# Optimization experiments

Hardware: AMD Instinct MI355X
Metric: run time of the kernel (lower is better)

The kernel has to match this reference:

```python
import jax, jax.numpy as jnp
import numpy as np

N = 100000          # nodes
E = 1600000         # edges (avg degree 16)
IN_DIM = 32
HID = 64
K = 2
XH = IN_DIM + HID   # 96, DiffConv input dim


def _xavier(key, shape):
    fan_in, fan_out = shape[-2], shape[-1]
    lim = float(np.sqrt(6.0 / (fan_in + fan_out)))
    return jax.random.uniform(key, shape, jnp.float32, -lim, lim)


def setup_inputs() -> dict:
    key = jax.random.key(0)
    ks = jax.random.split(key, 8)
    x = jax.random.normal(ks[0], (N, IN_DIM), jnp.float32)
    h = jax.random.normal(ks[1], (N, HID), jnp.float32)
    edge_index = jax.random.randint(ks[2], (2, E), 0, N, dtype=jnp.int32)
    edge_weight = jax.random.uniform(ks[3], (E,), jnp.float32)
    # stacked per-hop linear weights for each gate: (K+1, XH, HID)
    Wr = _xavier(ks[4], (K + 1, XH, HID))
    Wz = _xavier(ks[5], (K + 1, XH, HID))
    Wc = _xavier(ks[6], (K + 1, XH, HID))
    br = jnp.zeros((HID,), jnp.float32)
    bz = jnp.zeros((HID,), jnp.float32)
    bc = jnp.zeros((HID,), jnp.float32)
    return {"x": x, "h": h, "edge_index": edge_index, "edge_weight": edge_weight,
            "Wr": Wr, "br": br, "Wz": Wz, "bz": bz, "Wc": Wc, "bc": bc}


def _diff_conv(x, src, dst, norm_w, W, b, n):
    # DC(X) = sum_k Linear_k(P^k X),  P = D^{-1} W (row-normalised)
    out = x @ W[0]
    x_k = x
    for k in range(1, W.shape[0]):
        msgs = norm_w[:, None] * x_k[src]                     # gather + scale (E, F)
        x_k = jax.ops.segment_sum(msgs, dst, num_segments=n)  # scatter-add (N, F)
        out = out + x_k @ W[k]
    return out + b


def reference(x, h, edge_index, edge_weight, Wr, br, Wz, bz, Wc, bc):
    n = x.shape[0]
    src, dst = edge_index[0], edge_index[1]
    # out-degree normalisation on source nodes (clamped at 1)
    out_deg = jax.ops.segment_sum(jnp.ones_like(edge_weight), src, num_segments=n)
    out_deg = jnp.maximum(out_deg, 1.0)
    norm_w = edge_weight / out_deg[src]
    xh = jnp.concatenate([x, h], axis=-1)
    r = jax.nn.sigmoid(_diff_conv(xh, src, dst, norm_w, Wr, br, n))
    z = jax.nn.sigmoid(_diff_conv(xh, src, dst, norm_w, Wz, bz, n))
    xrh = jnp.concatenate([x, r * h], axis=-1)
    c = jnp.tanh(_diff_conv(xrh, src, dst, norm_w, Wc, bc, n))
    return z * h + (1.0 - z) * c
```

## Files before the change

kernel.cpp:

```cpp
#include <hip/hip_runtime.h>
#include <math.h>

#define NN 100000
#define NE 1600000
#define ECAP 64
#define GN 64
#define WSTR 296
#define LSTR 104

#define EPB 4096
#define NBLKA 391
#define BINB 256
#define NBINS 391
#define BCAP 4736

typedef __attribute__((ext_vector_type(4))) float f32x4;
typedef __attribute__((ext_vector_type(8))) short s16x8;

__device__ __forceinline__ unsigned int bfbits(float v) {
  unsigned int b = __float_as_uint(v);
  b += 0x7fffu + ((b >> 16) & 1u);
  return b >> 16;
}
__device__ __forceinline__ float bflo(unsigned int v) { return __uint_as_float(v << 16); }
__device__ __forceinline__ float bfhi(unsigned int v) { return __uint_as_float(v & 0xffff0000u); }
__device__ __forceinline__ uint4 pack8(float4 a, float4 b) {
  return make_uint4(bfbits(a.x) | (bfbits(a.y) << 16), bfbits(a.z) | (bfbits(a.w) << 16),
                    bfbits(b.x) | (bfbits(b.y) << 16), bfbits(b.z) | (bfbits(b.w) << 16));
}

__global__ __launch_bounds__(256) void k_binA(const int* __restrict__ src,
                                              const int* __restrict__ dst,
                                              const float* __restrict__ ew,
                                              int* __restrict__ gcur1,
                                              int* __restrict__ gcur2,
                                              int2* __restrict__ rec1,
                                              unsigned char* __restrict__ rec2) {
  __shared__ int h1[NBINS], h2[NBINS];
  int tid = threadIdx.x;
  for (int t = tid; t < NBINS; t += 256) { h1[t] = 0; h2[t] = 0; }
  __syncthreads();
  int base = blockIdx.x * EPB;
  int end = base + EPB; if (end > NE) end = NE;
  for (int e = base + tid; e < end; e += 256) {
    atomicAdd(&h1[dst[e] >> 8], 1);
    atomicAdd(&h2[src[e] >> 8], 1);
  }
  __syncthreads();
  for (int t = tid; t < NBINS; t += 256) {
    int c1 = h1[t];
    h1[t] = t * BCAP + (c1 ? atomicAdd(&gcur1[t], c1) : 0);
    int c2 = h2[t];
    h2[t] = t * BCAP + (c2 ? atomicAdd(&gcur2[t], c2) : 0);
  }
  __syncthreads();
  for (int e = base + tid; e < end; e += 256) {
    int d = dst[e], s = src[e];
    int p1 = atomicAdd(&h1[d >> 8], 1);
    rec1[p1] = make_int2(s | ((d & 255) << 20), __float_as_int(ew[e]));
    int p2 = atomicAdd(&h2[s >> 8], 1);
    rec2[p2] = (unsigned char)(s & 255);
  }
}

__global__ __launch_bounds__(256) void k_bdeg(const int* __restrict__ gcur2,
                                              const unsigned char* __restrict__ rec2,
                                              int* __restrict__ deg_out) {
  __shared__ int lc[BINB];
  int b = blockIdx.x, tid = threadIdx.x;
  lc[tid] = 0;
  __syncthreads();
  int cnt = gcur2[b];
  const unsigned char* rp = rec2 + (size_t)b * BCAP;
  for (int i = tid; i < cnt; i += 256) atomicAdd(&lc[rp[i]], 1);
  __syncthreads();
  int node = b * 256 + tid;
  if (node < NN) deg_out[node] = lc[tid];
}

__global__ __launch_bounds__(256) void k_bell(const int* __restrict__ gcur1,
                                              const int2* __restrict__ rec1,
                                              const int* __restrict__ deg_out,
                                              int2* __restrict__ ell,
                                              int* __restrict__ cursor) {
  __shared__ int lc[BINB];
  int b = blockIdx.x, tid = threadIdx.x;
  lc[tid] = 0;
  __syncthreads();
  int cnt = gcur1[b];
  const int2* rp = rec1 + (size_t)b * BCAP;
  for (int i = tid; i < cnt; i += 256) {
    int2 r = rp[i];
    int s = r.x & 0xFFFFF;
    int dl = (r.x >> 20) & 255;
    float w = __int_as_float(r.y) / fmaxf((float)deg_out[s], 1.0f);
    int p = atomicAdd(&lc[dl], 1);
    if (p < ECAP)
      ell[(size_t)(b * 256 + dl) * ECAP + p] = make_int2(s, __float_as_int(w));
  }
  __syncthreads();
  int node = b * 256 + tid;
  if (node < NN) cursor[node] = lc[tid];
}

__global__ __launch_bounds__(256) void k_xh0(const float* __restrict__ x,
                                             const float* __restrict__ h,
                                             unsigned int* __restrict__ xh0) {
  int idx = blockIdx.x * 256 + threadIdx.x;
  if (idx >= NN * 48) return;
  int n = idx / 48, c = idx - n * 48;
  float v0, v1;
  if (c < 16) {
    v0 = x[(size_t)n * 32 + 2 * c];
    v1 = x[(size_t)n * 32 + 2 * c + 1];
  } else {
    v0 = h[(size_t)n * 64 + 2 * (c - 16)];
    v1 = h[(size_t)n * 64 + 2 * (c - 16) + 1];
  }
  xh0[idx] = bfbits(v0) | (bfbits(v1) << 16);
}

__global__ __launch_bounds__(256) void k_wprep(const float* __restrict__ Wr,
                                               const float* __restrict__ Wz,
                                               const float* __restrict__ Wc,
                                               unsigned short* __restrict__ wt_rz,
                                               unsigned short* __restrict__ wt_c) {
  int idx = blockIdx.x * 256 + threadIdx.x;
  if (idx >= 192 * 36) return;
  int col = idx % 192;
  int k0 = (idx / 192) * 8;
  unsigned int packed[4];
#pragma unroll
  for (int p = 0; p < 4; ++p) {
    unsigned int lo, hi;
#pragma unroll
    for (int e = 0; e < 2; ++e) {
      int k = k0 + p * 2 + e;
      int t = k / 96, kl = k - t * 96;
      float v;
      if (col < 64) v = Wr[t * 6144 + kl * 64 + col];
      else if (col < 128) v = Wz[t * 6144 + kl * 64 + (col - 64)];
      else v = Wc[t * 6144 + kl * 64 + (col - 128)];
      if (e == 0) lo = bfbits(v); else hi = bfbits(v);
    }
    packed[p] = lo | (hi << 16);
  }
  unsigned short* dstp = (col < 128) ? (wt_rz + col * WSTR + k0)
                                     : (wt_c + (col - 128) * WSTR + k0);
  *reinterpret_cast<uint4*>(dstp) =
      make_uint4(packed[0], packed[1], packed[2], packed[3]);
}

__global__ __launch_bounds__(256) void k_prop96e(const uint2* __restrict__ in,
                                                 uint2* __restrict__ out,
                                                 const int* __restrict__ cnt_arr,
                                                 const int2* __restrict__ ell) {
  int hw = (blockIdx.x * 256 + threadIdx.x) >> 5;
  int lane = threadIdx.x & 31;
  if (hw >= NN) return;
  int cnt = cnt_arr[hw];
  if (cnt > ECAP) cnt = ECAP;
  const int2* ep = ell + (size_t)hw * ECAP;
  bool act = lane < 24;
  float a0 = 0.f, a1 = 0.f, a2 = 0.f, a3 = 0.f;
  float b0 = 0.f, b1 = 0.f, b2 = 0.f, b3 = 0.f;
  int i = 0;
  for (; i + 4 <= cnt; i += 4) {
    int2 e0 = ep[i], e1 = ep[i + 1], e2 = ep[i + 2], e3 = ep[i + 3];
    if (act) {
      uint2 v0 = in[(size_t)e0.x * 24 + lane];
      uint2 v1 = in[(size_t)e1.x * 24 + lane];
      uint2 v2 = in[(size_t)e2.x * 24 + lane];
      uint2 v3 = in[(size_t)e3.x * 24 + lane];
      float w0 = __int_as_float(e0.y), w1 = __int_as_float(e1.y);
      float w2 = __int_as_float(e2.y), w3 = __int_as_float(e3.y);
      a0 = fmaf(w0, bflo(v0.x), a0); a1 = fmaf(w0, bfhi(v0.x), a1);
      a2 = fmaf(w0, bflo(v0.y), a2); a3 = fmaf(w0, bfhi(v0.y), a3);
      b0 = fmaf(w1, bflo(v1.x), b0); b1 = fmaf(w1, bfhi(v1.x), b1);
      b2 = fmaf(w1, bflo(v1.y), b2); b3 = fmaf(w1, bfhi(v1.y), b3);
      a0 = fmaf(w2, bflo(v2.x), a0); a1 = fmaf(w2, bfhi(v2.x), a1);
      a2 = fmaf(w2, bflo(v2.y), a2); a3 = fmaf(w2, bfhi(v2.y), a3);
      b0 = fmaf(w3, bflo(v3.x), b0); b1 = fmaf(w3, bfhi(v3.x), b1);
      b2 = fmaf(w3, bflo(v3.y), b2); b3 = fmaf(w3, bfhi(v3.y), b3);
    }
  }
  for (; i < cnt; ++i) {
    int2 e = ep[i];
    if (act) {
      uint2 v = in[(size_t)e.x * 24 + lane];
      float w = __int_as_float(e.y);
      a0 = fmaf(w, bflo(v.x), a0); a1 = fmaf(w, bfhi(v.x), a1);
      a2 = fmaf(w, bflo(v.y), a2); a3 = fmaf(w, bfhi(v.y), a3);
    }
  }
  if (act) {
    uint2 o;
    o.x = bfbits(a0 + b0) | (bfbits(a1 + b1) << 16);
    o.y = bfbits(a2 + b2) | (bfbits(a3 + b3) << 16);
    out[(size_t)hw * 24 + lane] = o;
  }
}

__global__ __launch_bounds__(256) void k_prop64e(const unsigned int* __restrict__ in,
                                                 unsigned int* __restrict__ out,
                                                 const int* __restrict__ cnt_arr,
                                                 const int2* __restrict__ ell) {
  int hw = (blockIdx.x * 256 + threadIdx.x) >> 5;
  int lane = threadIdx.x & 31;
  if (hw >= NN) return;
  int cnt = cnt_arr[hw];
  if (cnt > ECAP) cnt = ECAP;
  const int2* ep = ell + (size_t)hw * ECAP;
  float a0 = 0.f, a1 = 0.f, b0 = 0.f, b1 = 0.f;
  int i = 0;
  for (; i + 4 <= cnt; i += 4) {
    int2 e0 = ep[i], e1 = ep[i + 1], e2 = ep[i + 2], e3 = ep[i + 3];
    unsigned int v0 = in[(size_t)e0.x * 32 + lane];
    unsigned int v1 = in[(size_t)e1.x * 32 + lane];
    unsigned int v2 = in[(size_t)e2.x * 32 + lane];
    unsigned int v3 = in[(size_t)e3.x * 32 + lane];
    float w0 = __int_as_float(e0.y), w1 = __int_as_float(e1.y);
    float w2 = __int_as_float(e2.y), w3 = __int_as_float(e3.y);
    a0 = fmaf(w0, bflo(v0), a0); a1 = fmaf(w0, bfhi(v0), a1);
    b0 = fmaf(w1, bflo(v1), b0); b1 = fmaf(w1, bfhi(v1), b1);
    a0 = fmaf(w2, bflo(v2), a0); a1 = fmaf(w2, bfhi(v2), a1);
    b0 = fmaf(w3, bflo(v3), b0); b1 = fmaf(w3, bfhi(v3), b1);
  }
  for (; i < cnt; ++i) {
    int2 e = ep[i];
    unsigned int v = in[(size_t)e.x * 32 + lane];
    float w = __int_as_float(e.y);
    a0 = fmaf(w, bflo(v), a0); a1 = fmaf(w, bfhi(v), a1);
  }
  out[(size_t)hw * 32 + lane] = bfbits(a0 + b0) | (bfbits(a1 + b1) << 16);
}

__device__ __forceinline__ void stage_f32f32(unsigned short* sA, int nb0,
                                             const float* __restrict__ srcA,
                                             const float* __restrict__ srcB) {
  for (int i = threadIdx.x; i < GN * 12; i += 256) {
    int n = i / 12, ch = i % 12;
    int g = nb0 + n;
    uint4 v = make_uint4(0, 0, 0, 0);
    if (g < NN) {
      if (ch < 4) {
        float4 f0 = *reinterpret_cast<const float4*>(srcA + (size_t)g * 32 + ch * 8);
        float4 f1 = *reinterpret_cast<const float4*>(srcA + (size_t)g * 32 + ch * 8 + 4);
        v = pack8(f0, f1);
      } else {
        float4 f0 = *reinterpret_cast<const float4*>(srcB + (size_t)g * 64 + (ch - 4) * 8);
        float4 f1 = *reinterpret_cast<const float4*>(srcB + (size_t)g * 64 + (ch - 4) * 8 + 4);
        v = pack8(f0, f1);
      }
    }
    *reinterpret_cast<uint4*>(&sA[n * LSTR + ch * 8]) = v;
  }
}

__device__ __forceinline__ void stage_copy96(unsigned short* sA, int nb0,
                                             const unsigned short* __restrict__ src) {
  for (int i = threadIdx.x; i < GN * 12; i += 256) {
    int n = i / 12, ch = i % 12;
    int g = nb0 + n;
    uint4 v = make_uint4(0, 0, 0, 0);
    if (g < NN) v = *reinterpret_cast<const uint4*>(src + (size_t)g * 96 + ch * 8);
    *reinterpret_cast<uint4*>(&sA[n * LSTR + ch * 8]) = v;
  }
}

__device__ __forceinline__ void stage_f32bf(unsigned short* sA, int nb0,
                                            const float* __restrict__ srcA,
                                            const unsigned short* __restrict__ srcB) {
  for (int i = threadIdx.x; i < GN * 12; i += 256) {
    int n = i / 12, ch = i % 12;
    int g = nb0 + n;
    uint4 v = make_uint4(0, 0, 0, 0);
    if (g < NN) {
      if (ch < 4) {
        float4 f0 = *reinterpret_cast<const float4*>(srcA + (size_t)g * 32 + ch * 8);
        float4 f1 = *reinterpret_cast<const float4*>(srcA + (size_t)g * 32 + ch * 8 + 4);
        v = pack8(f0, f1);
      } else {
        v = *reinterpret_cast<const uint4*>(srcB + (size_t)g * 64 + (ch - 4) * 8);
      }
    }
    *reinterpret_cast<uint4*>(&sA[n * LSTR + ch * 8]) = v;
  }
}

__device__ __forceinline__ void stage_bfbf(unsigned short* sA, int nb0,
                                           const unsigned short* __restrict__ srcA,
                                           const unsigned short* __restrict__ srcB) {
  for (int i = threadIdx.x; i < GN * 12; i += 256) {
    int n = i / 12, ch = i % 12;
    int g = nb0 + n;
    uint4 v = make_uint4(0, 0, 0, 0);
    if (g < NN) {
      if (ch < 4) v = *reinterpret_cast<const uint4*>(srcA + (size_t)g * 96 + ch * 8);
      else v = *reinterpret_cast<const uint4*>(srcB + (size_t)g * 64 + (ch - 4) * 8);
    }
    *reinterpret_cast<uint4*>(&sA[n * LSTR + ch * 8]) = v;
  }
}

template <int NCOLS>
__device__ __forceinline__ void stage_w(unsigned short* sW,
                                        const unsigned short* __restrict__ wt, int t) {
  for (int i = threadIdx.x; i < NCOLS * 12; i += 256) {
    int col = i / 12, ch = i % 12;
    uint4 v = *reinterpret_cast<const uint4*>(wt + col * WSTR + t * 96 + ch * 8);
    *reinterpret_cast<uint4*>(&sW[col * LSTR + ch * 8]) = v;
  }
}

__global__ __launch_bounds__(256) void k_rz(const float* __restrict__ x,
                                            const float* __restrict__ h,
                                            const unsigned short* __restrict__ xh1,
                                            const unsigned short* __restrict__ xh2,
                                            const unsigned short* __restrict__ wt_rz,
                                            const float* __restrict__ br,
                                            const float* __restrict__ bz,
                                            unsigned short* __restrict__ rh,
                                            float* __restrict__ zb) {
  __shared__ alignas(16) unsigned short sA[GN * LSTR];
  __shared__ alignas(16) unsigned short sW[128 * LSTR];
  int tid = threadIdx.x;
  int nb0 = blockIdx.x * GN;
  int wv = tid >> 6, l = tid & 63;
  int l15 = l & 15, lg = l >> 4;
  int n0 = wv * 32;

  f32x4 acc[4][2];
#pragma unroll
  for (int nt = 0; nt < 2; ++nt) {
    int colc = n0 + nt * 16 + l15;
    float bias = (colc < 64) ? br[colc] : bz[colc - 64];
#pragma unroll
    for (int mt = 0; mt < 4; ++mt) acc[mt][nt] = {bias, bias, bias, bias};
  }

#pragma unroll
  for (int t = 0; t < 3; ++t) {
    if (t == 0) stage_f32f32(sA, nb0, x, h);
    else if (t == 1) stage_copy96(sA, nb0, xh1);
    else stage_copy96(sA, nb0, xh2);
    stage_w<128>(sW, wt_rz, t);
    __syncthreads();
#pragma unroll
    for (int ks = 0; ks < 3; ++ks) {
      int kb = ks * 32 + lg * 8;
      s16x8 af[4];
#pragma unroll
      for (int mt = 0; mt < 4; ++mt)
        af[mt] = *reinterpret_cast<const s16x8*>(&sA[(mt * 16 + l15) * LSTR + kb]);
      s16x8 bf0 = *reinterpret_cast<const s16x8*>(&sW[(n0 + l15) * LSTR + kb]);
      s16x8 bf1 = *reinterpret_cast<const s16x8*>(&sW[(n0 + 16 + l15) * LSTR + kb]);
#pragma unroll
      for (int mt = 0; mt < 4; ++mt) {
        acc[mt][0] = __builtin_amdgcn_mfma_f32_16x16x32_bf16(af[mt], bf0, acc[mt][0], 0, 0, 0);
        acc[mt][1] = __builtin_amdgcn_mfma_f32_16x16x32_bf16(af[mt], bf1, acc[mt][1], 0, 0, 0);
      }
    }
    __syncthreads();
  }

#pragma unroll
  for (int mt = 0; mt < 4; ++mt) {
#pragma unroll
    for (int nt = 0; nt < 2; ++nt) {
      int colc = n0 + nt * 16 + l15;
#pragma unroll
      for (int r = 0; r < 4; ++r) {
        int g = nb0 + mt * 16 + lg * 4 + r;
        if (g < NN) {
          float pre = acc[mt][nt][r];
          float sg = 1.f / (1.f + expf(-pre));
          if (colc < 64) {
            float hv = h[(size_t)g * 64 + colc];
            rh[(size_t)g * 64 + colc] = (unsigned short)bfbits(sg * hv);
          } else {
            zb[(size_t)g * 64 + (colc - 64)] = sg;
          }
        }
      }
    }
  }
}

__global__ __launch_bounds__(256) void k_c(const float* __restrict__ x,
                                           const float* __restrict__ h,
                                           const unsigned short* __restrict__ rhf,
                                           const unsigned short* __restrict__ xh1,
                                           const unsigned short* __restrict__ xh2,
                                           const unsigned short* __restrict__ rh1,
                                           const unsigned short* __restrict__ rh2,
                                           const unsigned short* __restrict__ wt_c,
                                           const float* __restrict__ bc,
                                           const float* __restrict__ zb,
                                           float* __restrict__ out) {
  __shared__ alignas(16) unsigned short sA[GN * LSTR];
  __shared__ alignas(16) unsigned short sW[64 * LSTR];
  int tid = threadIdx.x;
  int nb0 = blockIdx.x * GN;
  int wv = tid >> 6, l = tid & 63;
  int l15 = l & 15, lg = l >> 4;
  int n0 = wv * 16;

  float bias = bc[n0 + l15];
  f32x4 acc[4];
#pragma unroll
  for (int mt = 0; mt < 4; ++mt) acc[mt] = {bias, bias, bias, bias};

#pragma unroll
  for (int t = 0; t < 3; ++t) {
    if (t == 0) stage_f32bf(sA, nb0, x, rhf);
    else if (t == 1) stage_bfbf(sA, nb0, xh1, rh1);
    else stage_bfbf(sA, nb0, xh2, rh2);
    stage_w<64>(sW, wt_c, t);
    __syncthreads();
#pragma unroll
    for (int ks = 0; ks < 3; ++ks) {
      int kb = ks * 32 + lg * 8;
      s16x8 bf0 = *reinterpret_cast<const s16x8*>(&sW[(n0 + l15) * LSTR + kb]);
#pragma unroll
      for (int mt = 0; mt < 4; ++mt) {
        s16x8 af = *reinterpret_cast<const s16x8*>(&sA[(mt * 16 + l15) * LSTR + kb]);
        acc[mt] = __builtin_amdgcn_mfma_f32_16x16x32_bf16(af, bf0, acc[mt], 0, 0, 0);
      }
    }
    __syncthreads();
  }

  int colc = n0 + l15;
#pragma unroll
  for (int mt = 0; mt < 4; ++mt) {
#pragma unroll
    for (int r = 0; r < 4; ++r) {
      int g = nb0 + mt * 16 + lg * 4 + r;
      if (g < NN) {
        float cv = tanhf(acc[mt][r]);
        float z = zb[(size_t)g * 64 + colc];
        float hv = h[(size_t)g * 64 + colc];
        out[(size_t)g * 64 + colc] = z * hv + (1.f - z) * cv;
      }
    }
  }
}

extern "C" void kernel_launch(void* const* d_in, const int* in_sizes, int n_in,
                              void* d_out, int out_size, void* d_ws, size_t ws_size,
                              hipStream_t stream) {
  const float* x = (const float*)d_in[0];
  const float* h = (const float*)d_in[1];
  const int* eidx = (const int*)d_in[2];
  const float* ew = (const float*)d_in[3];
  const float* Wr = (const float*)d_in[4];
  const float* br = (const float*)d_in[5];
  const float* Wz = (const float*)d_in[6];
  const float* bz = (const float*)d_in[7];
  const float* Wc = (const float*)d_in[8];
  const float* bc = (const float*)d_in[9];
  const int* src = eidx;
  const int* dst = eidx + NE;
  float* out = (float*)d_out;

  int* ip = (int*)d_ws;
  int* gcur1 = ip;
  int* gcur2 = ip + 512;
  int* deg_out = ip + 1024;
  int* cursor = deg_out + NN;
  int2* rec1 = (int2*)(cursor + NN);
  unsigned char* rec2 = (unsigned char*)(rec1 + (size_t)NBINS * BCAP);
  int2* ell = (int2*)(rec2 + ((size_t)NBINS * BCAP + 8) / 8 * 8);
  float* zb = (float*)(ell + (size_t)NN * ECAP);
  unsigned short* xh0 = (unsigned short*)(zb + (size_t)NN * 64);
  unsigned short* xh1 = xh0 + (size_t)NN * 96;
  unsigned short* xh2 = xh1 + (size_t)NN * 96;
  unsigned short* rh  = xh2 + (size_t)NN * 96;
  unsigned short* rh1 = rh + (size_t)NN * 64;
  unsigned short* rh2 = rh1 + (size_t)NN * 64;
  unsigned short* wt_rz = rh2 + (size_t)NN * 64;
  unsigned short* wt_c = wt_rz + 128 * WSTR;

  hipMemsetAsync(ip, 0, 1024 * sizeof(int), stream);

  dim3 blk(256);
  k_wprep<<<dim3((192 * 36 + 255) / 256), blk, 0, stream>>>(Wr, Wz, Wc, wt_rz, wt_c);
  k_binA<<<dim3(NBLKA), blk, 0, stream>>>(src, dst, ew, gcur1, gcur2, rec1, rec2);
  k_bdeg<<<dim3(NBINS), blk, 0, stream>>>(gcur2, rec2, deg_out);
  k_bell<<<dim3(NBINS), blk, 0, stream>>>(gcur1, rec1, deg_out, ell, cursor);
  k_xh0<<<dim3(NN * 48 / 256), blk, 0, stream>>>(x, h, (unsigned int*)xh0);

  k_prop96e<<<dim3(NN / 8), blk, 0, stream>>>((const uint2*)xh0, (uint2*)xh1,
                                              cursor, ell);
  k_prop96e<<<dim3(NN / 8), blk, 0, stream>>>((const uint2*)xh1, (uint2*)xh2,
                                              cursor, ell);
  k_rz<<<dim3((NN + GN - 1) / GN), blk, 0, stream>>>(x, h, xh1, xh2, wt_rz, br, bz, rh, zb);
  k_prop64e<<<dim3(NN / 8), blk, 0, stream>>>((const unsigned int*)rh,
                                              (unsigned int*)rh1, cursor, ell);
  k_prop64e<<<dim3(NN / 8), blk, 0, stream>>>((const unsigned int*)rh1,
                                              (unsigned int*)rh2, cursor, ell);
  k_c<<<dim3((NN + GN - 1) / GN), blk, 0, stream>>>(x, h, rh, xh1, xh2, rh1, rh2,
                                                    wt_c, bc, zb, out);
}
```

Before: 426.7 us.

## Read bf16 xh0 and weights directly from global, store z gate in bf16

The gate kernels now stage the precomputed bf16 xh0 buffer instead of re-reading and converting fp32 x and h. Weight fragments are loaded straight from global memory (cached) instead of being staged into shared memory, which drops the sW arrays and lowers LDS use. The z gate is stored as bf16, halving its write and read traffic. The final blend now uses bf16-rounded h and z values, which adds precision loss, and the direct weight loads rely on the cache to keep latency down.

Result: faster. 387.5 us (-9.2%).

```diff
diff --git a/kernel.cpp b/kernel.cpp
--- a/kernel.cpp
+++ b/kernel.cpp
@@ -24,10 +24,7 @@
 }
 __device__ __forceinline__ float bflo(unsigned int v) { return __uint_as_float(v << 16); }
 __device__ __forceinline__ float bfhi(unsigned int v) { return __uint_as_float(v & 0xffff0000u); }
-__device__ __forceinline__ uint4 pack8(float4 a, float4 b) {
-  return make_uint4(bfbits(a.x) | (bfbits(a.y) << 16), bfbits(a.z) | (bfbits(a.w) << 16),
-                    bfbits(b.x) | (bfbits(b.y) << 16), bfbits(b.z) | (bfbits(b.w) << 16));
-}
+__device__ __forceinline__ float bf1(unsigned short v) { return __uint_as_float((unsigned int)v << 16); }
 
 __global__ __launch_bounds__(256) void k_binA(const int* __restrict__ src,
                                               const int* __restrict__ dst,
@@ -235,28 +232,6 @@
   out[(size_t)hw * 32 + lane] = bfbits(a0 + b0) | (bfbits(a1 + b1) << 16);
 }
 
-__device__ __forceinline__ void stage_f32f32(unsigned short* sA, int nb0,
-                                             const float* __restrict__ srcA,
-                                             const float* __restrict__ srcB) {
-  for (int i = threadIdx.x; i < GN * 12; i += 256) {
-    int n = i / 12, ch = i % 12;
-    int g = nb0 + n;
-    uint4 v = make_uint4(0, 0, 0, 0);
-    if (g < NN) {
-      if (ch < 4) {
-        float4 f0 = *reinterpret_cast<const float4*>(srcA + (size_t)g * 32 + ch * 8);
-        float4 f1 = *reinterpret_cast<const float4*>(srcA + (size_t)g * 32 + ch * 8 + 4);
-        v = pack8(f0, f1);
-      } else {
-        float4 f0 = *reinterpret_cast<const float4*>(srcB + (size_t)g * 64 + (ch - 4) * 8);
-        float4 f1 = *reinterpret_cast<const float4*>(srcB + (size_t)g * 64 + (ch - 4) * 8 + 4);
-        v = pack8(f0, f1);
-      }
-    }
-    *reinterpret_cast<uint4*>(&sA[n * LSTR + ch * 8]) = v;
-  }
-}
-
 __device__ __forceinline__ void stage_copy96(unsigned short* sA, int nb0,
                                              const unsigned short* __restrict__ src) {
   for (int i = threadIdx.x; i < GN * 12; i += 256) {
@@ -264,26 +239,6 @@
     int g = nb0 + n;
     uint4 v = make_uint4(0, 0, 0, 0);
     if (g < NN) v = *reinterpret_cast<const uint4*>(src + (size_t)g * 96 + ch * 8);
-    *reinterpret_cast<uint4*>(&sA[n * LSTR + ch * 8]) = v;
-  }
-}
-
-__device__ __forceinline__ void stage_f32bf(unsigned short* sA, int nb0,
-                                            const float* __restrict__ srcA,
-                                            const unsigned short* __restrict__ srcB) {
-  for (int i = threadIdx.x; i < GN * 12; i += 256) {
-    int n = i / 12, ch = i % 12;
-    int g = nb0 + n;
-    uint4 v = make_uint4(0, 0, 0, 0);
-    if (g < NN) {
-      if (ch < 4) {
-        float4 f0 = *reinterpret_cast<const float4*>(srcA + (size_t)g * 32 + ch * 8);
-        float4 f1 = *reinterpret_cast<const float4*>(srcA + (size_t)g * 32 + ch * 8 + 4);
-        v = pack8(f0, f1);
-      } else {
-        v = *reinterpret_cast<const uint4*>(srcB + (size_t)g * 64 + (ch - 4) * 8);
-      }
-    }
     *reinterpret_cast<uint4*>(&sA[n * LSTR + ch * 8]) = v;
   }
 }
@@ -303,27 +258,15 @@
   }
 }
 
-template <int NCOLS>
-__device__ __forceinline__ void stage_w(unsigned short* sW,
-                                        const unsigned short* __restrict__ wt, int t) {
-  for (int i = threadIdx.x; i < NCOLS * 12; i += 256) {
-    int col = i / 12, ch = i % 12;
-    uint4 v = *reinterpret_cast<const uint4*>(wt + col * WSTR + t * 96 + ch * 8);
-    *reinterpret_cast<uint4*>(&sW[col * LSTR + ch * 8]) = v;
-  }
-}
-
-__global__ __launch_bounds__(256) void k_rz(const float* __restrict__ x,
-                                            const float* __restrict__ h,
+__global__ __launch_bounds__(256) void k_rz(const unsigned short* __restrict__ xh0,
                                             const unsigned short* __restrict__ xh1,
                                             const unsigned short* __restrict__ xh2,
                                             const unsigned short* __restrict__ wt_rz,
                                             const float* __restrict__ br,
                                             const float* __restrict__ bz,
                                             unsigned short* __restrict__ rh,
-                                            float* __restrict__ zb) {
+                                            unsigned short* __restrict__ zbb) {
   __shared__ alignas(16) unsigned short sA[GN * LSTR];
-  __shared__ alignas(16) unsigned short sW[128 * LSTR];
   int tid = threadIdx.x;
   int nb0 = blockIdx.x * GN;
   int wv = tid >> 6, l = tid & 63;
@@ -339,26 +282,25 @@
     for (int mt = 0; mt < 4; ++mt) acc[mt][nt] = {bias, bias, bias, bias};
   }
 
+  const unsigned short* w0p = wt_rz + (size_t)(n0 + l15) * WSTR + lg * 8;
+  const unsigned short* w1p = wt_rz + (size_t)(n0 + 16 + l15) * WSTR + lg * 8;
+
 #pragma unroll
   for (int t = 0; t < 3; ++t) {
-    if (t == 0) stage_f32f32(sA, nb0, x, h);
+    if (t == 0) stage_copy96(sA, nb0, xh0);
     else if (t == 1) stage_copy96(sA, nb0, xh1);
     else stage_copy96(sA, nb0, xh2);
-    stage_w<128>(sW, wt_rz, t);
     __syncthreads();
 #pragma unroll
     for (int ks = 0; ks < 3; ++ks) {
       int kb = ks * 32 + lg * 8;
-      s16x8 af[4];
-#pragma unroll
-      for (int mt = 0; mt < 4; ++mt)
-        af[mt] = *reinterpret_cast<const s16x8*>(&sA[(mt * 16 + l15) * LSTR + kb]);
-      s16x8 bf0 = *reinterpret_cast<const s16x8*>(&sW[(n0 + l15) * LSTR + kb]);
-      s16x8 bf1 = *reinterpret_cast<const s16x8*>(&sW[(n0 + 16 + l15) * LSTR + kb]);
+      s16x8 bf0 = *reinterpret_cast<const s16x8*>(w0p + t * 96 + ks * 32);
+      s16x8 bf1 = *reinterpret_cast<const s16x8*>(w1p + t * 96 + ks * 32);
 #pragma unroll
       for (int mt = 0; mt < 4; ++mt) {
-        acc[mt][0] = __builtin_amdgcn_mfma_f32_16x16x32_bf16(af[mt], bf0, acc[mt][0], 0, 0, 0);
-        acc[mt][1] = __builtin_amdgcn_mfma_f32_16x16x32_bf16(af[mt], bf1, acc[mt][1], 0, 0, 0);
+        s16x8 af = *reinterpret_cast<const s16x8*>(&sA[(mt * 16 + l15) * LSTR + kb]);
+        acc[mt][0] = __builtin_amdgcn_mfma_f32_16x16x32_bf16(af, bf0, acc[mt][0], 0, 0, 0);
+        acc[mt][1] = __builtin_amdgcn_mfma_f32_16x16x32_bf16(af, bf1, acc[mt][1], 0, 0, 0);
       }
     }
     __syncthreads();
@@ -376,10 +318,10 @@
           float pre = acc[mt][nt][r];
           float sg = 1.f / (1.f + expf(-pre));
           if (colc < 64) {
-            float hv = h[(size_t)g * 64 + colc];
+            float hv = bf1(xh0[(size_t)g * 96 + 32 + colc]);
             rh[(size_t)g * 64 + colc] = (unsigned short)bfbits(sg * hv);
           } else {
-            zb[(size_t)g * 64 + (colc - 64)] = sg;
+            zbb[(size_t)g * 64 + (colc - 64)] = (unsigned short)bfbits(sg);
           }
         }
       }
@@ -387,8 +329,7 @@
   }
 }
 
-__global__ __launch_bounds__(256) void k_c(const float* __restrict__ x,
-                                           const float* __restrict__ h,
+__global__ __launch_bounds__(256) void k_c(const unsigned short* __restrict__ xh0,
                                            const unsigned short* __restrict__ rhf,
                                            const unsigned short* __restrict__ xh1,
                                            const unsigned short* __restrict__ xh2,
@@ -396,10 +337,9 @@
                                            const unsigned short* __restrict__ rh2,
                                            const unsigned short* __restrict__ wt_c,
                                            const float* __restrict__ bc,
-                                           const float* __restrict__ zb,
+                                           const unsigned short* __restrict__ zbb,
                                            float* __restrict__ out) {
   __shared__ alignas(16) unsigned short sA[GN * LSTR];
-  __shared__ alignas(16) unsigned short sW[64 * LSTR];
   int tid = threadIdx.x;
   int nb0 = blockIdx.x * GN;
   int wv = tid >> 6, l = tid & 63;
@@ -411,17 +351,18 @@
 #pragma unroll
   for (int mt = 0; mt < 4; ++mt) acc[mt] = {bias, bias, bias, bias};
 
+  const unsigned short* wp = wt_c + (size_t)(n0 + l15) * WSTR + lg * 8;
+
 #pragma unroll
   for (int t = 0; t < 3; ++t) {
-    if (t == 0) stage_f32bf(sA, nb0, x, rhf);
+    if (t == 0) stage_bfbf(sA, nb0, xh0, rhf);
     else if (t == 1) stage_bfbf(sA, nb0, xh1, rh1);
     else stage_bfbf(sA, nb0, xh2, rh2);
-    stage_w<64>(sW, wt_c, t);
     __syncthreads();
 #pragma unroll
     for (int ks = 0; ks < 3; ++ks) {
       int kb = ks * 32 + lg * 8;
-      s16x8 bf0 = *reinterpret_cast<const s16x8*>(&sW[(n0 + l15) * LSTR + kb]);
+      s16x8 bf0 = *reinterpret_cast<const s16x8*>(wp + t * 96 + ks * 32);
 #pragma unroll
       for (int mt = 0; mt < 4; ++mt) {
         s16x8 af = *reinterpret_cast<const s16x8*>(&sA[(mt * 16 + l15) * LSTR + kb]);
@@ -439,8 +380,8 @@
       int g = nb0 + mt * 16 + lg * 4 + r;
       if (g < NN) {
         float cv = tanhf(acc[mt][r]);
-        float z = zb[(size_t)g * 64 + colc];
-        float hv = h[(size_t)g * 64 + colc];
+        float z = bf1(zbb[(size_t)g * 64 + colc]);
+        float hv = bf1(xh0[(size_t)g * 96 + 32 + colc]);
         out[(size_t)g * 64 + colc] = z * hv + (1.f - z) * cv;
       }
     }
@@ -472,8 +413,8 @@
   int2* rec1 = (int2*)(cursor + NN);
   unsigned char* rec2 = (unsigned char*)(rec1 + (size_t)NBINS * BCAP);
   int2* ell = (int2*)(rec2 + ((size_t)NBINS * BCAP + 8) / 8 * 8);
-  float* zb = (float*)(ell + (size_t)NN * ECAP);
-  unsigned short* xh0 = (unsigned short*)(zb + (size_t)NN * 64);
+  unsigned short* zbb = (unsigned short*)(ell + (size_t)NN * ECAP);
+  unsigned short* xh0 = zbb + (size_t)NN * 64;
   unsigned short* xh1 = xh0 + (size_t)NN * 96;
   unsigned short* xh2 = xh1 + (size_t)NN * 96;
   unsigned short* rh  = xh2 + (size_t)NN * 96;
@@ -495,11 +436,11 @@
                                               cursor, ell);
   k_prop96e<<<dim3(NN / 8), blk, 0, stream>>>((const uint2*)xh1, (uint2*)xh2,
                                               cursor, ell);
-  k_rz<<<dim3((NN + GN - 1) / GN), blk, 0, stream>>>(x, h, xh1, xh2, wt_rz, br, bz, rh, zb);
+  k_rz<<<dim3((NN + GN - 1) / GN), blk, 0, stream>>>(xh0, xh1, xh2, wt_rz, br, bz, rh, zbb);
   k_prop64e<<<dim3(NN / 8), blk, 0, stream>>>((const unsigned int*)rh,
                                               (unsigned int*)rh1, cursor, ell);
   k_prop64e<<<dim3(NN / 8), blk, 0, stream>>>((const unsigned int*)rh1,
                                               (unsigned int*)rh2, cursor, ell);
-  k_c<<<dim3((NN + GN - 1) / GN), blk, 0, stream>>>(x, h, rh, xh1, xh2, rh1, rh2,
-                                                    wt_c, bc, zb, out);
-}
+  k_c<<<dim3((NN + GN - 1) / GN), blk, 0, stream>>>(xh0, rh, xh1, xh2, rh1, rh2,
+                                                    wt_c, bc, zbb, out);
+}
```
